# Performance work log

Hardware: AMD Instinct MI355X
Metric: run time of the kernel (lower is better)

## Reference

```python
import jax, jax.numpy as jnp
import numpy as np

N_NODES, D, B, NEG2, DRUG_NUM = 20000, 512, 2048, 64, 2000
H1, H2 = 128, 64


def setup_inputs() -> dict:
    ks = jax.random.split(jax.random.key(0), 10)
    embed = jax.random.normal(ks[0], (N_NODES, D), dtype=jnp.float32)
    h = jax.random.randint(ks[1], (B, 1), 0, DRUG_NUM)
    t = jax.random.randint(ks[2], (B, 1), 0, N_NODES)
    n_s = jax.random.randint(ks[3], (B, NEG2), 0, DRUG_NUM)  # all < drug_num -> chunk branch
    s1 = 1.0 / np.sqrt(2 * D)
    s2 = 1.0 / np.sqrt(H1)
    s3 = 1.0 / np.sqrt(H2)
    W1 = jax.random.uniform(ks[4], (2 * D, H1), minval=-s1, maxval=s1, dtype=jnp.float32)
    b1 = jax.random.uniform(ks[5], (H1,), minval=-s1, maxval=s1, dtype=jnp.float32)
    W2 = jax.random.uniform(ks[6], (H1, H2), minval=-s2, maxval=s2, dtype=jnp.float32)
    b2 = jax.random.uniform(ks[7], (H2,), minval=-s2, maxval=s2, dtype=jnp.float32)
    W3 = jax.random.uniform(ks[8], (H2, 1), minval=-s3, maxval=s3, dtype=jnp.float32)
    b3 = jax.random.uniform(ks[9], (1,), minval=-s3, maxval=s3, dtype=jnp.float32)
    return {"embed": embed, "W1": W1, "b1": b1, "W2": W2, "b2": b2, "W3": W3, "b3": b3,
            "h": h, "t": t, "n_s": n_s}


def _mlp(x, W1, b1, W2, b2, W3, b3):
    # [..., 2D] -> [...] score
    x = jax.nn.relu(x @ W1 + b1)
    x = jax.nn.relu(x @ W2 + b2)
    return (x @ W3 + b3)[..., 0]


def reference(embed, W1, b1, W2, b2, W3, b3, h, t, n_s):
    K = n_s.shape[1] // 2
    n_t, n_h = n_s[:, :K], n_s[:, K:]
    h_e = embed[h]          # [B, 1, D]
    t_e = embed[t]          # [B, T, D]
    T = t.shape[1]
    # positive pairs: [B, T]
    pos = _mlp(jnp.concatenate([jnp.tile(h_e, (1, T, 1)), t_e], axis=-1),
               W1, b1, W2, b2, W3, b3)
    # corrupted-tail negatives: [B, K]
    neg1 = _mlp(jnp.concatenate([jnp.tile(h_e, (1, K, 1)), embed[n_t]], axis=-1),
                W1, b1, W2, b2, W3, b3)
    # corrupted-head negatives: [B, T*K] (T=1 here)
    neg2 = _mlp(jnp.concatenate([embed[n_h], jnp.tile(t_e, (1, K, 1))], axis=-1),
                W1, b1, W2, b2, W3, b3)
    neg = jnp.concatenate([neg1, neg2], axis=1)  # [B, 2K]
    return pos, neg
```

## Files before the change

### kernel.cpp

```cpp
#include <hip/hip_runtime.h>

#define DIM    512
#define BATCH  2048
#define NDRUG  2000
#define H1     128
#define H2     64
#define NITEM  65
#define SLAB   774144
#define W2F_OFF  (SLAB)
#define W1F_OFF  (W2F_OFF + 4096)
#define LP       65

typedef __attribute__((ext_vector_type(8))) short short8;
typedef __attribute__((ext_vector_type(4))) float floatx4;

__device__ inline unsigned f2bf(float x) {
    union { float f; unsigned u; } v; v.f = x;
    unsigned r = v.u + 0x7fffu + ((v.u >> 16) & 1u);
    return r >> 16;
}
__device__ inline unsigned pkbf(float a, float b) {
    return f2bf(a) | (f2bf(b) << 16);
}
__device__ inline short8 cvt8(const float* __restrict__ src) {
    float4 a = *(const float4*)src, b = *(const float4*)(src + 4);
    union { short8 s; unsigned u[4]; } v;
    v.u[0] = pkbf(a.x, a.y); v.u[1] = pkbf(a.z, a.w);
    v.u[2] = pkbf(b.x, b.y); v.u[3] = pkbf(b.z, b.w);
    return v.s;
}

__global__ __launch_bounds__(256) void pack_w(
    const float* __restrict__ W1, const float* __restrict__ W2,
    float* __restrict__ ws)
{
    const int blk = blockIdx.x, tid = threadIdx.x;
    if (blk < 64) {
        short8* W1f = (short8*)(ws + W1F_OFF);
        int item = blk * 256 + tid;
        int frag = item >> 6, fl = item & 63;
        int half = frag >> 7, rem = frag & 127;
        int nt = rem >> 4, kt = rem & 15;
        int fn = fl & 15, fq = fl >> 4;
        short8 v;
        #pragma unroll
        for (int j = 0; j < 8; ++j) {
            int k = half * DIM + kt * 32 + fq * 8 + j;
            v[j] = (short)f2bf(W1[k * H1 + nt * 16 + fn]);
        }
        W1f[item] = v;
    } else {
        short8* W2f = (short8*)(ws + W2F_OFF);
        #pragma unroll
        for (int i = 0; i < 4; ++i) {
            int item = i * 256 + tid;
            int frag = item >> 6, fl = item & 63;
            int kt = frag >> 2, nt = frag & 3;
            int fn = fl & 15, fq = fl >> 4;
            short8 v;
            #pragma unroll
            for (int j = 0; j < 8; ++j)
                v[j] = (short)f2bf(W2[(kt * 32 + fq * 8 + j) * H2 + nt * 16 + fn]);
            W2f[item] = v;
        }
    }
}

template<int NT>
__device__ inline void l1_core(const short8* __restrict__ Wh,
                               const short8* __restrict__ ldsA,
                               int n, int q, int lane, floatx4* acc)
{
    short8 B[2][NT * 4];
    #pragma unroll
    for (int i = 0; i < NT; ++i)
        #pragma unroll
        for (int k = 0; k < 4; ++k)
            B[0][i * 4 + k] = Wh[(i * 16 + k) * 64 + lane];

    #pragma unroll
    for (int g = 0; g < 4; ++g) {
        const int cur = g & 1, nxt = cur ^ 1;
        if (g < 3) {
            #pragma unroll
            for (int i = 0; i < NT; ++i)
                #pragma unroll
                for (int k = 0; k < 4; ++k)
                    B[nxt][i * 4 + k] = Wh[(i * 16 + (g + 1) * 4 + k) * 64 + lane];
        }
        #pragma unroll
        for (int k = 0; k < 4; ++k) {
            short8 a = ldsA[n * LP + (g * 4 + k) * 4 + q];
            #pragma unroll
            for (int i = 0; i < NT; ++i)
                acc[i] = __builtin_amdgcn_mfma_f32_16x16x32_bf16(
                             a, B[cur][i * 4 + k], acc[i], 0, 0, 0);
        }
    }
}

__global__ __launch_bounds__(256) void layer1_k(
    const float* __restrict__ embed, const float* __restrict__ b1,
    const int* __restrict__ t, float* __restrict__ ws)
{
    __shared__ short8 ldsA[16 * LP];
    const short8* W1f = (const short8*)(ws + W1F_OFF);
    const int blk = blockIdx.x, tid = threadIdx.x;
    const bool isPQ = blk < 125;
    const int rowbase = isPQ ? blk * 16 : (blk - 125) * 16;
    const int lane = tid & 63, wv = tid >> 6;
    const int n = lane & 15, q = lane >> 4;

    #pragma unroll
    for (int i = 0; i < 4; ++i) {
        int u = i * 256 + tid;
        int r = u >> 6, c = u & 63;
        size_t grow = isPQ ? (size_t)(rowbase + r) : (size_t)t[rowbase + r];
        ldsA[r * LP + c] = cvt8(embed + grow * DIM + c * 8);
    }
    __syncthreads();

    if (isPQ) {
        const int T0 = wv * 4;
        const int half = (T0 >= 8) ? 1 : 0;
        const int ntbase = T0 & 7;
        floatx4 acc[4];
        #pragma unroll
        for (int i = 0; i < 4; ++i) acc[i] = (floatx4){0.f, 0.f, 0.f, 0.f};
        const short8* Wh = W1f + (size_t)((half * 8 + ntbase) * 16) * 64;
        l1_core<4>(Wh, ldsA, n, q, lane, acc);
        float* tbl = ws + (half ? NDRUG * H1 : 0);
        #pragma unroll
        for (int i = 0; i < 4; ++i) {
            int nt = ntbase + i;
            float badd = half ? b1[nt * 16 + n] : 0.f;
            #pragma unroll
            for (int reg = 0; reg < 4; ++reg)
                tbl[(size_t)(rowbase + q * 4 + reg) * H1 + nt * 16 + n] =
                    acc[i][reg] + badd;
        }
    } else {
        const int ntbase = wv * 2;
        floatx4 acc[2];
        #pragma unroll
        for (int i = 0; i < 2; ++i) acc[i] = (floatx4){0.f, 0.f, 0.f, 0.f};
        const short8* Wh = W1f + (size_t)((8 + ntbase) * 16) * 64;
        l1_core<2>(Wh, ldsA, n, q, lane, acc);
        float* tbl = ws + 2 * (NDRUG * H1);
        #pragma unroll
        for (int i = 0; i < 2; ++i) {
            int nt = ntbase + i;
            float badd = b1[nt * 16 + n];
            #pragma unroll
            for (int reg = 0; reg < 4; ++reg)
                tbl[(size_t)(rowbase + q * 4 + reg) * H1 + nt * 16 + n] =
                    acc[i][reg] + badd;
        }
    }
}

__global__ __launch_bounds__(256) void score_k(
    const float* __restrict__ ws,
    const float* __restrict__ b2, const float* __restrict__ W3,
    const float* __restrict__ b3,
    const int* __restrict__ h, const int* __restrict__ ns,
    float* __restrict__ out)
{
    __shared__ short8 w2lds[1024];
    const float* P  = ws;
    const float* Q  = ws + NDRUG * H1;
    const float* Qt = Q + NDRUG * H1;
    const short8* W2f = (const short8*)(ws + W2F_OFF);

    const int tid = threadIdx.x;
    const int lane = tid & 63, wv = tid >> 6;
    const int tile = blockIdx.x * 4 + wv;
    const int n = lane & 15, q = lane >> 4;

    const int sg   = tile * 16 + n;
    const int b    = sg / NITEM;
    const int item = sg - b * NITEM;
    const bool midQ = (item >= 1 && item <= 32);
    const int rowA = (item <= 32) ? h[b] : ns[b * 64 + 32 + (item - 33)];
    const int rowB = midQ ? ns[b * 64 + item - 1] : b;

    #pragma unroll
    for (int i = 0; i < 4; ++i)
        w2lds[i * 256 + tid] = W2f[i * 256 + tid];
    __syncthreads();

    const float* Pr = P + (size_t)rowA * H1;
    const float* Qr = (midQ ? Q : Qt) + (size_t)rowB * H1;

    float4 pr[8], qr[8];
    #pragma unroll
    for (int kt = 0; kt < 4; ++kt) {
        const int kb = kt * 32 + q * 8;
        pr[kt * 2]     = *(const float4*)(Pr + kb);
        pr[kt * 2 + 1] = *(const float4*)(Pr + kb + 4);
        qr[kt * 2]     = *(const float4*)(Qr + kb);
        qr[kt * 2 + 1] = *(const float4*)(Qr + kb + 4);
    }

    floatx4 acc[4];
    #pragma unroll
    for (int nt = 0; nt < 4; ++nt) acc[nt] = (floatx4){0.f, 0.f, 0.f, 0.f};

    #pragma unroll
    for (int kt = 0; kt < 4; ++kt) {
        float4 p0 = pr[kt * 2], p1 = pr[kt * 2 + 1];
        float4 q0 = qr[kt * 2], q1 = qr[kt * 2 + 1];
        union { short8 s; unsigned u[4]; } A;
        A.u[0] = pkbf(fmaxf(p0.x + q0.x, 0.f), fmaxf(p0.y + q0.y, 0.f));
        A.u[1] = pkbf(fmaxf(p0.z + q0.z, 0.f), fmaxf(p0.w + q0.w, 0.f));
        A.u[2] = pkbf(fmaxf(p1.x + q1.x, 0.f), fmaxf(p1.y + q1.y, 0.f));
        A.u[3] = pkbf(fmaxf(p1.z + q1.z, 0.f), fmaxf(p1.w + q1.w, 0.f));
        #pragma unroll
        for (int nt = 0; nt < 4; ++nt) {
            short8 bf = w2lds[(kt * 4 + nt) * 64 + lane];
            acc[nt] = __builtin_amdgcn_mfma_f32_16x16x32_bf16(A.s, bf, acc[nt], 0, 0, 0);
        }
    }

    float part[4];
    #pragma unroll
    for (int reg = 0; reg < 4; ++reg) {
        float sum = 0.f;
        #pragma unroll
        for (int nt = 0; nt < 4; ++nt) {
            int j = nt * 16 + n;
            sum = fmaf(fmaxf(acc[nt][reg] + b2[j], 0.f), W3[j], sum);
        }
        part[reg] = sum;
    }
    #pragma unroll
    for (int m = 1; m < 16; m <<= 1) {
        #pragma unroll
        for (int reg = 0; reg < 4; ++reg)
            part[reg] += __shfl_xor(part[reg], m, 64);
    }
    if (n == 0) {
        const float base3 = b3[0];
        #pragma unroll
        for (int reg = 0; reg < 4; ++reg) {
            int gid = tile * 16 + q * 4 + reg;
            int bb  = gid / NITEM;
            int it  = gid - bb * NITEM;
            float val = part[reg] + base3;
            if (it == 0) out[bb] = val;
            else         out[BATCH + bb * 64 + (it - 1)] = val;
        }
    }
}

extern "C" void kernel_launch(void* const* d_in, const int* in_sizes, int n_in,
                              void* d_out, int out_size, void* d_ws, size_t ws_size,
                              hipStream_t stream) {
    const float* embed = (const float*)d_in[0];
    const float* W1    = (const float*)d_in[1];
    const float* b1    = (const float*)d_in[2];
    const float* W2    = (const float*)d_in[3];
    const float* b2    = (const float*)d_in[4];
    const float* W3    = (const float*)d_in[5];
    const float* b3    = (const float*)d_in[6];
    const int*   h     = (const int*)d_in[7];
    const int*   t     = (const int*)d_in[8];
    const int*   ns    = (const int*)d_in[9];
    float* out = (float*)d_out;
    float* ws  = (float*)d_ws;

    pack_w<<<65, 256, 0, stream>>>(W1, W2, ws);
    layer1_k<<<253, 256, 0, stream>>>(embed, b1, t, ws);
    score_k<<<(BATCH * NITEM) / 64, 256, 0, stream>>>(ws, b2, W3, b3,
                                                      h, ns, out);
}
```

Baseline: 114.6 us.

## Process four tiles per wave in score kernel with double-buffered row prefetch

Each wave in the score kernel now handles four 16-item tiles instead of one, so the grid shrinks from 2080 to 520 blocks. The gathered P/Q rows for the next tile are loaded while the current tile's MFMA and reduction run. This spreads the per-block W2 LDS staging over more work and hides gather latency, at the cost of more registers per wave (launch bounds now ask for 2 blocks per CU) and fewer blocks to fill the GPU.

```diff
diff --git a/kernel.cpp b/kernel.cpp
--- a/kernel.cpp
+++ b/kernel.cpp
@@ -159,7 +159,7 @@
     }
 }
 
-__global__ __launch_bounds__(256) void score_k(
+__global__ __launch_bounds__(256, 2) void score_k(
     const float* __restrict__ ws,
     const float* __restrict__ b2, const float* __restrict__ W3,
     const float* __restrict__ b3,
@@ -174,81 +174,103 @@
 
     const int tid = threadIdx.x;
     const int lane = tid & 63, wv = tid >> 6;
-    const int tile = blockIdx.x * 4 + wv;
+    const int tbase = blockIdx.x * 16 + wv * 4;
     const int n = lane & 15, q = lane >> 4;
 
-    const int sg   = tile * 16 + n;
-    const int b    = sg / NITEM;
-    const int item = sg - b * NITEM;
-    const bool midQ = (item >= 1 && item <= 32);
-    const int rowA = (item <= 32) ? h[b] : ns[b * 64 + 32 + (item - 33)];
-    const int rowB = midQ ? ns[b * 64 + item - 1] : b;
+    int rowA[4], rowB[4]; bool midQ[4];
+    #pragma unroll
+    for (int i = 0; i < 4; ++i) {
+        int sg   = (tbase + i) * 16 + n;
+        int b    = sg / NITEM;
+        int item = sg - b * NITEM;
+        midQ[i] = (item >= 1 && item <= 32);
+        rowA[i] = (item <= 32) ? h[b] : ns[b * 64 + 32 + (item - 33)];
+        rowB[i] = midQ[i] ? ns[b * 64 + item - 1] : b;
+    }
 
     #pragma unroll
     for (int i = 0; i < 4; ++i)
         w2lds[i * 256 + tid] = W2f[i * 256 + tid];
     __syncthreads();
 
-    const float* Pr = P + (size_t)rowA * H1;
-    const float* Qr = (midQ ? Q : Qt) + (size_t)rowB * H1;
-
-    float4 pr[8], qr[8];
-    #pragma unroll
-    for (int kt = 0; kt < 4; ++kt) {
-        const int kb = kt * 32 + q * 8;
-        pr[kt * 2]     = *(const float4*)(Pr + kb);
-        pr[kt * 2 + 1] = *(const float4*)(Pr + kb + 4);
-        qr[kt * 2]     = *(const float4*)(Qr + kb);
-        qr[kt * 2 + 1] = *(const float4*)(Qr + kb + 4);
-    }
-
-    floatx4 acc[4];
-    #pragma unroll
-    for (int nt = 0; nt < 4; ++nt) acc[nt] = (floatx4){0.f, 0.f, 0.f, 0.f};
-
-    #pragma unroll
-    for (int kt = 0; kt < 4; ++kt) {
-        float4 p0 = pr[kt * 2], p1 = pr[kt * 2 + 1];
-        float4 q0 = qr[kt * 2], q1 = qr[kt * 2 + 1];
-        union { short8 s; unsigned u[4]; } A;
-        A.u[0] = pkbf(fmaxf(p0.x + q0.x, 0.f), fmaxf(p0.y + q0.y, 0.f));
-        A.u[1] = pkbf(fmaxf(p0.z + q0.z, 0.f), fmaxf(p0.w + q0.w, 0.f));
-        A.u[2] = pkbf(fmaxf(p1.x + q1.x, 0.f), fmaxf(p1.y + q1.y, 0.f));
-        A.u[3] = pkbf(fmaxf(p1.z + q1.z, 0.f), fmaxf(p1.w + q1.w, 0.f));
-        #pragma unroll
-        for (int nt = 0; nt < 4; ++nt) {
-            short8 bf = w2lds[(kt * 4 + nt) * 64 + lane];
-            acc[nt] = __builtin_amdgcn_mfma_f32_16x16x32_bf16(A.s, bf, acc[nt], 0, 0, 0);
-        }
-    }
-
-    float part[4];
-    #pragma unroll
-    for (int reg = 0; reg < 4; ++reg) {
-        float sum = 0.f;
-        #pragma unroll
-        for (int nt = 0; nt < 4; ++nt) {
-            int j = nt * 16 + n;
-            sum = fmaf(fmaxf(acc[nt][reg] + b2[j], 0.f), W3[j], sum);
-        }
-        part[reg] = sum;
-    }
-    #pragma unroll
-    for (int m = 1; m < 16; m <<= 1) {
-        #pragma unroll
-        for (int reg = 0; reg < 4; ++reg)
-            part[reg] += __shfl_xor(part[reg], m, 64);
-    }
-    if (n == 0) {
-        const float base3 = b3[0];
+    float4 pr[2][8], qr[2][8];
+    {
+        const float* Pr = P + (size_t)rowA[0] * H1;
+        const float* Qr = (midQ[0] ? Q : Qt) + (size_t)rowB[0] * H1;
+        #pragma unroll
+        for (int kt = 0; kt < 4; ++kt) {
+            const int kb = kt * 32 + q * 8;
+            pr[0][kt * 2]     = *(const float4*)(Pr + kb);
+            pr[0][kt * 2 + 1] = *(const float4*)(Pr + kb + 4);
+            qr[0][kt * 2]     = *(const float4*)(Qr + kb);
+            qr[0][kt * 2 + 1] = *(const float4*)(Qr + kb + 4);
+        }
+    }
+
+    const float base3 = b3[0];
+    #pragma unroll
+    for (int i = 0; i < 4; ++i) {
+        const int cur = i & 1, nxt = cur ^ 1;
+        if (i < 3) {
+            const float* Pr = P + (size_t)rowA[i + 1] * H1;
+            const float* Qr = (midQ[i + 1] ? Q : Qt) + (size_t)rowB[i + 1] * H1;
+            #pragma unroll
+            for (int kt = 0; kt < 4; ++kt) {
+                const int kb = kt * 32 + q * 8;
+                pr[nxt][kt * 2]     = *(const float4*)(Pr + kb);
+                pr[nxt][kt * 2 + 1] = *(const float4*)(Pr + kb + 4);
+                qr[nxt][kt * 2]     = *(const float4*)(Qr + kb);
+                qr[nxt][kt * 2 + 1] = *(const float4*)(Qr + kb + 4);
+            }
+        }
+
+        floatx4 acc[4];
+        #pragma unroll
+        for (int nt = 0; nt < 4; ++nt) acc[nt] = (floatx4){0.f, 0.f, 0.f, 0.f};
+
+        #pragma unroll
+        for (int kt = 0; kt < 4; ++kt) {
+            float4 p0 = pr[cur][kt * 2], p1 = pr[cur][kt * 2 + 1];
+            float4 q0 = qr[cur][kt * 2], q1 = qr[cur][kt * 2 + 1];
+            union { short8 s; unsigned u[4]; } A;
+            A.u[0] = pkbf(fmaxf(p0.x + q0.x, 0.f), fmaxf(p0.y + q0.y, 0.f));
+            A.u[1] = pkbf(fmaxf(p0.z + q0.z, 0.f), fmaxf(p0.w + q0.w, 0.f));
+            A.u[2] = pkbf(fmaxf(p1.x + q1.x, 0.f), fmaxf(p1.y + q1.y, 0.f));
+            A.u[3] = pkbf(fmaxf(p1.z + q1.z, 0.f), fmaxf(p1.w + q1.w, 0.f));
+            #pragma unroll
+            for (int nt = 0; nt < 4; ++nt) {
+                short8 bf = w2lds[(kt * 4 + nt) * 64 + lane];
+                acc[nt] = __builtin_amdgcn_mfma_f32_16x16x32_bf16(A.s, bf, acc[nt], 0, 0, 0);
+            }
+        }
+
+        float part[4];
         #pragma unroll
         for (int reg = 0; reg < 4; ++reg) {
-            int gid = tile * 16 + q * 4 + reg;
-            int bb  = gid / NITEM;
-            int it  = gid - bb * NITEM;
-            float val = part[reg] + base3;
-            if (it == 0) out[bb] = val;
-            else         out[BATCH + bb * 64 + (it - 1)] = val;
+            float sum = 0.f;
+            #pragma unroll
+            for (int nt = 0; nt < 4; ++nt) {
+                int j = nt * 16 + n;
+                sum = fmaf(fmaxf(acc[nt][reg] + b2[j], 0.f), W3[j], sum);
+            }
+            part[reg] = sum;
+        }
+        #pragma unroll
+        for (int m = 1; m < 16; m <<= 1) {
+            #pragma unroll
+            for (int reg = 0; reg < 4; ++reg)
+                part[reg] += __shfl_xor(part[reg], m, 64);
+        }
+        if (n == 0) {
+            #pragma unroll
+            for (int reg = 0; reg < 4; ++reg) {
+                int gid = (tbase + i) * 16 + q * 4 + reg;
+                int bb  = gid / NITEM;
+                int it  = gid - bb * NITEM;
+                float val = part[reg] + base3;
+                if (it == 0) out[bb] = val;
+                else         out[BATCH + bb * 64 + (it - 1)] = val;
+            }
         }
     }
 }
@@ -271,6 +293,5 @@
 
     pack_w<<<65, 256, 0, stream>>>(W1, W2, ws);
     layer1_k<<<253, 256, 0, stream>>>(embed, b1, t, ws);
-    score_k<<<(BATCH * NITEM) / 64, 256, 0, stream>>>(ws, b2, W3, b3,
-                                                      h, ns, out);
-}
+    score_k<<<520, 256, 0, stream>>>(ws, b2, W3, b3, h, ns, out);
+}
```

After: 116.4 us. Within noise of the previous version (+1.5%).
